# Performance work log

Measured on AMD Instinct MI355X. Metric: run time of the kernel, lower is better.

Reference implementation:

```python
import jax, jax.numpy as jnp
import numpy as np

COMMITMENT_COST = 0.25


def setup_inputs() -> dict:
    key = jax.random.key(0)
    k1, k2 = jax.random.split(key)
    z_e = jax.random.normal(k1, (32, 64, 64, 64), dtype=jnp.float32)  # [B, C, H, W]
    emb = jax.random.normal(k2, (1024, 64), dtype=jnp.float32)        # [K, D] codebook
    return {"z_e": z_e, "emb": emb}


def reference(z_e, emb):
    B, C, H, W = z_e.shape
    K, D = emb.shape
    # [B, C, H, W] -> [B, H, W, C] -> [N, D]
    z = jnp.transpose(z_e, (0, 2, 3, 1))
    z_flat = z.reshape(-1, D)
    # squared L2 distances: ||z||^2 + ||e||^2 - 2 z e^T  -> [N, K]
    distances = (jnp.sum(z_flat * z_flat, axis=1, keepdims=True)
                 + jnp.sum(emb * emb, axis=1)
                 - 2.0 * (z_flat @ emb.T))
    indices = jnp.argmin(distances, axis=1)               # [N]
    encodings = jax.nn.one_hot(indices, K, dtype=z_flat.dtype)  # [N, K]
    quantized = emb[indices].reshape(z.shape)             # [B, H, W, D]
    # commitment loss (codebook is frozen / EMA-updated, so quantized is detached)
    loss = COMMITMENT_COST * jnp.mean((jax.lax.stop_gradient(quantized) - z) ** 2)
    # straight-through estimator
    quantized_st = z + jax.lax.stop_gradient(quantized - z)
    avg_probs = jnp.mean(encodings, axis=0)               # [K]
    perplexity = jnp.exp(-jnp.sum(avg_probs * jnp.log(avg_probs + 1e-10)))
    out = jnp.transpose(quantized_st, (0, 3, 1, 2))       # back to [B, C, H, W]
    return out, loss, perplexity, encodings
```

## Files before the change

kernel.cpp:

```cpp
#include <hip/hip_runtime.h>

typedef __attribute__((ext_vector_type(8)))  __bf16 bf16x8;
typedef __attribute__((ext_vector_type(16))) float  f32x16;

#define NPTS   131072
#define KCODES 1024
#define DDIM   64
#define HWSZ   4096

#define LOSS_OFF    8388608
#define PERP_OFF    8388609
#define ENC_OFF     8388610

#define IMG_BYTES   25600
#define HIST_OFF    409600
#define BLOSS_OFF   413696
#define WS_NEED     415744

#define GLOBAL_AS __attribute__((address_space(1)))
#define LDS_AS    __attribute__((address_space(3)))

__device__ __forceinline__ unsigned rnhi(float x) {
    unsigned u = __float_as_uint(x);
    return (u + 0x7fffu + ((u >> 16) & 1u)) & 0xffff0000u;
}

__device__ __forceinline__ void split3(float x, unsigned short& h1, unsigned short& h2, unsigned short& h3) {
    unsigned a = rnhi(x); float r1 = x - __uint_as_float(a);
    unsigned b = rnhi(r1); float r2 = r1 - __uint_as_float(b);
    unsigned c = rnhi(r2);
    h1 = (unsigned short)(a >> 16);
    h2 = (unsigned short)(b >> 16);
    h3 = (unsigned short)(c >> 16);
}

__global__ __launch_bounds__(256) void prep_kernel(const float* __restrict__ emb,
                                                   uint4* __restrict__ planes,
                                                   int* __restrict__ hist) {
    const int k = blockIdx.x * 256 + threadIdx.x;
    hist[k] = 0;
    float row[DDIM];
    const float4* r = (const float4*)(emb + (size_t)k * DDIM);
    float s0 = 0.f, s1 = 0.f, s2 = 0.f, s3 = 0.f;
#pragma unroll
    for (int i = 0; i < 16; ++i) {
        float4 v = r[i];
        row[4 * i + 0] = v.x; row[4 * i + 1] = v.y;
        row[4 * i + 2] = v.z; row[4 * i + 3] = v.w;
        s0 = fmaf(v.x, v.x, s0);
        s1 = fmaf(v.y, v.y, s1);
        s2 = fmaf(v.z, v.z, s2);
        s3 = fmaf(v.w, v.w, s3);
    }
    const float e2v = (s0 + s1) + (s2 + s3);

    const int c  = k >> 6, lc = k & 63;
    uint4* img = planes + (size_t)c * (IMG_BYTES / 16);
#pragma unroll
    for (int sl = 0; sl < 8; ++sl) {
        unsigned w1[4], w2[4], w3[4];
#pragma unroll
        for (int m = 0; m < 4; ++m) {
            unsigned short a0, b0, c0, a1, b1, c1;
            split3(-2.f * row[sl * 8 + 2 * m    ], a0, b0, c0);
            split3(-2.f * row[sl * 8 + 2 * m + 1], a1, b1, c1);
            w1[m] = (unsigned)a0 | ((unsigned)a1 << 16);
            w2[m] = (unsigned)b0 | ((unsigned)b1 << 16);
            w3[m] = (unsigned)c0 | ((unsigned)c1 << 16);
        }
        img[0 * 512 + sl * 64 + lc] = make_uint4(w1[0], w1[1], w1[2], w1[3]);
        img[1 * 512 + sl * 64 + lc] = make_uint4(w2[0], w2[1], w2[2], w2[3]);
        img[2 * 512 + sl * 64 + lc] = make_uint4(w3[0], w3[1], w3[2], w3[3]);
    }
    {
        unsigned short s1e, s2e, s3e;
        split3(e2v, s1e, s2e, s3e);
        img[1536 + lc] = make_uint4((unsigned)s1e | ((unsigned)s2e << 16), (unsigned)s3e, 0u, 0u);
    }
}

__global__ __launch_bounds__(512, 4) void vq_fused(
    const float* __restrict__ z_e, const char* __restrict__ planesg,
    const float* __restrict__ emb, float* __restrict__ out,
    float* __restrict__ enc, int* __restrict__ hist,
    float* __restrict__ blockLoss)
{
    __shared__ __align__(16) char sbuf[2][IMG_BYTES];
    __shared__ int   sidx[256];
    __shared__ float swsum[8];

    const int tid  = threadIdx.x, bid = blockIdx.x;
    const int lane = tid & 63,    wid = tid >> 6;
    const int hi   = lane >> 5,   col = lane & 31;

    {
#pragma unroll
        for (int i = 0; i < 4; ++i) {
            const int seg = wid + 8 * i;
            if (seg < 25) {
                const char* g = planesg + seg * 1024 + lane * 16;
                __builtin_amdgcn_global_load_lds((const GLOBAL_AS void*)g,
                                                 (LDS_AS void*)(&sbuf[0][0] + seg * 1024), 16, 0, 0);
            }
        }
    }

    float* encSlice = enc + (size_t)bid * 256 * KCODES;
    float4* encF4   = (float4*)(encSlice + 2);

    const int n  = bid * 256 + wid * 32 + col;
    const int b  = n >> 12, hw = n & (HWSZ - 1);
    const float* zp = z_e + (size_t)b * (DDIM * HWSZ) + hw;

    bf16x8 Bv0[4], Bv1[4], Bv2[4];
    float zzp = 0.f;
#pragma unroll
    for (int kk = 0; kk < 4; ++kk) {
        union { unsigned u[4]; bf16x8 v; } p1, p2, p3;
#pragma unroll
        for (int m = 0; m < 4; ++m) {
            float x0 = zp[(size_t)(16 * kk + 8 * hi + 2 * m    ) * HWSZ];
            float x1 = zp[(size_t)(16 * kk + 8 * hi + 2 * m + 1) * HWSZ];
            zzp = fmaf(x0, x0, zzp);
            zzp = fmaf(x1, x1, zzp);
            unsigned short a0, b0, c0, a1, b1, c1;
            split3(x0, a0, b0, c0);
            split3(x1, a1, b1, c1);
            p1.u[m] = (unsigned)a0 | ((unsigned)a1 << 16);
            p2.u[m] = (unsigned)b0 | ((unsigned)b1 << 16);
            p3.u[m] = (unsigned)c0 | ((unsigned)c1 << 16);
        }
        Bv0[kk] = p1.v; Bv1[kk] = p2.v; Bv2[kk] = p3.v;
    }

    bf16x8 Bone;
    {
        union { unsigned u[4]; bf16x8 v; } o;
        o.u[0] = hi ? 0u : 0x3F803F80u;
        o.u[1] = hi ? 0u : 0x00003F80u;
        o.u[2] = 0u; o.u[3] = 0u;
        Bone = o.v;
    }

    __syncthreads();

    float best = 3.4e38f;
    int   bestk = 0;
    const float4 z4 = make_float4(0.f, 0.f, 0.f, 0.f);

    for (int c = 0; c < 16; ++c) {
        const int cur = c & 1;
        if (c + 1 < 16) {
            const char* gimg = planesg + (size_t)(c + 1) * IMG_BYTES;
#pragma unroll
            for (int i = 0; i < 4; ++i) {
                const int seg = wid + 8 * i;
                if (seg < 25) {
                    __builtin_amdgcn_global_load_lds((const GLOBAL_AS void*)(gimg + seg * 1024 + lane * 16),
                                                     (LDS_AS void*)(&sbuf[1 - cur][0] + seg * 1024), 16, 0, 0);
                }
            }
        }
        {
            const int base = c * 4096 + tid;
#pragma unroll
            for (int j = 0; j < 8; ++j) {
                const int idx = base + j * 512;
                if (idx < 65535) encF4[idx] = z4;
            }
            if (c == 0) {
                if (tid == 0) *(float2*)encSlice = make_float2(0.f, 0.f);
                if (tid == 1) *(float2*)(encSlice + 262142) = make_float2(0.f, 0.f);
            }
        }

        const char* img = &sbuf[cur][0];
#pragma unroll
        for (int t = 0; t < 2; ++t) {
            const int rowoff = (32 * t + col) * 16;
            f32x16 acc = {0.f,0.f,0.f,0.f,0.f,0.f,0.f,0.f,0.f,0.f,0.f,0.f,0.f,0.f,0.f,0.f};
            bf16x8 eA = *(const bf16x8*)(img + 24576 + rowoff);
            acc = __builtin_amdgcn_mfma_f32_32x32x16_bf16(eA, Bone, acc, 0, 0, 0);
#pragma unroll
            for (int kk = 0; kk < 4; ++kk) {
                const char* bse = img + (2 * kk + hi) * 1024 + rowoff;
                bf16x8 a1 = *(const bf16x8*)(bse);
                bf16x8 a2 = *(const bf16x8*)(bse + 8192);
                acc = __builtin_amdgcn_mfma_f32_32x32x16_bf16(a1, Bv0[kk], acc, 0, 0, 0);
                acc = __builtin_amdgcn_mfma_f32_32x32x16_bf16(a2, Bv0[kk], acc, 0, 0, 0);
                acc = __builtin_amdgcn_mfma_f32_32x32x16_bf16(a1, Bv1[kk], acc, 0, 0, 0);
                acc = __builtin_amdgcn_mfma_f32_32x32x16_bf16(a2, Bv1[kk], acc, 0, 0, 0);
                bf16x8 a3 = *(const bf16x8*)(bse + 16384);
                acc = __builtin_amdgcn_mfma_f32_32x32x16_bf16(a3, Bv0[kk], acc, 0, 0, 0);
                acc = __builtin_amdgcn_mfma_f32_32x32x16_bf16(a1, Bv2[kk], acc, 0, 0, 0);
            }
            const int cbase = c * 64 + 32 * t + 4 * hi;
#pragma unroll
            for (int r = 0; r < 16; ++r) {
                const int code = cbase + (r & 3) + 8 * (r >> 2);
                const float sc = acc[r];
                if (sc < best) { best = sc; bestk = code; }
            }
        }
        __syncthreads();
    }

    float obest = __shfl_down(best, 32);
    int   oidx  = __shfl_down(bestk, 32);
    float ozz   = __shfl_down(zzp, 32);
    if (obest < best || (obest == best && oidx < bestk)) { best = obest; bestk = oidx; }
    const float zz = zzp + ozz;
    float contrib = (lane < 32) ? (best + zz) : 0.f;
    if (lane < 32) {
        sidx[wid * 32 + col] = bestk;
        atomicAdd(&hist[bestk], 1);
    }
#pragma unroll
    for (int off = 32; off > 0; off >>= 1) contrib += __shfl_down(contrib, off);
    if (lane == 0) swsum[wid] = contrib;
    __syncthreads();
    if (tid == 0) {
        float s = 0.f;
        for (int i = 0; i < 8; ++i) s += swsum[i];
        blockLoss[bid] = s;
    }

    if (lane < 32) {
        const int nn = bid * 256 + wid * 32 + col;
        enc[(size_t)nn * KCODES + bestk] = 1.0f;
    }

    {
        const int i  = tid & 255, c0 = (tid >> 8) * 32;
        const int k  = sidx[i];
        const int nn = bid * 256 + i, bb = nn >> 12, hh = nn & (HWSZ - 1);
        const float4* er = (const float4*)(emb + (size_t)k * DDIM + c0);
        float* ob = out + (size_t)bb * (DDIM * HWSZ) + hh;
#pragma unroll
        for (int m = 0; m < 8; ++m) {
            float4 q = er[m];
            ob[(size_t)(c0 + 4 * m    ) * HWSZ] = q.x;
            ob[(size_t)(c0 + 4 * m + 1) * HWSZ] = q.y;
            ob[(size_t)(c0 + 4 * m + 2) * HWSZ] = q.z;
            ob[(size_t)(c0 + 4 * m + 3) * HWSZ] = q.w;
        }
    }
}

__global__ __launch_bounds__(256) void e2_kernel(const float* __restrict__ emb,
                                                 float* __restrict__ e2,
                                                 int* __restrict__ hist) {
    int k = blockIdx.x * 256 + threadIdx.x;
    hist[k] = 0;
    const float4* r = (const float4*)(emb + (size_t)k * DDIM);
    float s0 = 0.f, s1 = 0.f, s2 = 0.f, s3 = 0.f;
#pragma unroll
    for (int i = 0; i < 16; ++i) {
        float4 v = r[i];
        s0 = fmaf(v.x, v.x, s0);
        s1 = fmaf(v.y, v.y, s1);
        s2 = fmaf(v.z, v.z, s2);
        s3 = fmaf(v.w, v.w, s3);
    }
    e2[k] = (s0 + s1) + (s2 + s3);
}

__global__ __launch_bounds__(512, 4) void vq_mfma(
    const float* __restrict__ z_e, const float* __restrict__ emb,
    const float* __restrict__ e2g, float* __restrict__ out,
    float* __restrict__ enc, int* __restrict__ hist,
    float* __restrict__ blockLoss)
{
    __shared__ unsigned short planeA[3 * 8 * 1024];
    __shared__ float se2[KCODES];
    __shared__ int   sidx[256];
    __shared__ float swsum[8];

    const int tid  = threadIdx.x, bid = blockIdx.x;
    const int lane = tid & 63,    wid = tid >> 6;
    const int hi   = lane >> 5,   col = lane & 31;

    for (int i = tid; i < KCODES; i += 512) se2[i] = e2g[i];

    float* encSlice = enc + (size_t)bid * 256 * KCODES;
    float4* encF4   = (float4*)(encSlice + 2);

    const int n  = bid * 256 + wid * 32 + col;
    const int b  = n >> 12, hw = n & (HWSZ - 1);
    const float* zp = z_e + (size_t)b * (DDIM * HWSZ) + hw;

    bf16x8 Bv[3][4];
    float zzp = 0.f;
#pragma unroll
    for (int kk = 0; kk < 4; ++kk) {
        union { unsigned u[4]; bf16x8 v; } p1, p2, p3;
#pragma unroll
        for (int m = 0; m < 4; ++m) {
            float x0 = zp[(size_t)(16 * kk + 8 * hi + 2 * m    ) * HWSZ];
            float x1 = zp[(size_t)(16 * kk + 8 * hi + 2 * m + 1) * HWSZ];
            zzp = fmaf(x0, x0, zzp);
            zzp = fmaf(x1, x1, zzp);
            unsigned short a0, b0, c0, a1, b1, c1;
            split3(x0, a0, b0, c0);
            split3(x1, a1, b1, c1);
            p1.u[m] = (unsigned)a0 | ((unsigned)a1 << 16);
            p2.u[m] = (unsigned)b0 | ((unsigned)b1 << 16);
            p3.u[m] = (unsigned)c0 | ((unsigned)c1 << 16);
        }
        Bv[0][kk] = p1.v; Bv[1][kk] = p2.v; Bv[2][kk] = p3.v;
    }

    float best = 3.4e38f;
    int   bestk = 0;

    for (int chunk = 0; chunk < 8; ++chunk) {
        __syncthreads();
#pragma unroll
        for (int it = 0; it < 2; ++it) {
            const int code = tid & 127;
            const int sl   = (tid >> 7) + 4 * it;
            const float4* ep = (const float4*)(emb + (size_t)(chunk * 128 + code) * DDIM + sl * 8);
            float4 va = ep[0], vb = ep[1];
            float xs[8] = {va.x, va.y, va.z, va.w, vb.x, vb.y, vb.z, vb.w};
            unsigned w1[4], w2[4], w3[4];
#pragma unroll
            for (int m = 0; m < 4; ++m) {
                unsigned short a0, b0, c0, a1, b1, c1;
                split3(-2.f * xs[2 * m    ], a0, b0, c0);
                split3(-2.f * xs[2 * m + 1], a1, b1, c1);
                w1[m] = (unsigned)a0 | ((unsigned)a1 << 16);
                w2[m] = (unsigned)b0 | ((unsigned)b1 << 16);
                w3[m] = (unsigned)c0 | ((unsigned)c1 << 16);
            }
            const int off = sl * 1024 + code * 8;
            *(uint4*)&planeA[0 * 8192 + off] = make_uint4(w1[0], w1[1], w1[2], w1[3]);
            *(uint4*)&planeA[1 * 8192 + off] = make_uint4(w2[0], w2[1], w2[2], w2[3]);
            *(uint4*)&planeA[2 * 8192 + off] = make_uint4(w3[0], w3[1], w3[2], w3[3]);
        }
        __syncthreads();

        {
            const float4 z4 = make_float4(0.f, 0.f, 0.f, 0.f);
            const int base = chunk * 8192 + tid;
#pragma unroll
            for (int it = 0; it < 16; ++it) {
                const int idx = base + it * 512;
                if (idx < 65535) encF4[idx] = z4;
            }
            if (chunk == 0) {
                if (tid == 0) *(float2*)encSlice = make_float2(0.f, 0.f);
                if (tid == 1) *(float2*)(encSlice + 262142) = make_float2(0.f, 0.f);
            }
        }

        for (int t = 0; t < 4; ++t) {
            f32x16 acc0 = {0.f,0.f,0.f,0.f,0.f,0.f,0.f,0.f,0.f,0.f,0.f,0.f,0.f,0.f,0.f,0.f};
            f32x16 acc1 = {0.f,0.f,0.f,0.f,0.f,0.f,0.f,0.f,0.f,0.f,0.f,0.f,0.f,0.f,0.f,0.f};
            const int arow = (32 * t + col) * 8;
#pragma unroll
            for (int kk = 0; kk < 4; ++kk) {
                const int sb = (2 * kk + hi) * 1024 + arow;
                bf16x8 a1 = *(const bf16x8*)&planeA[0 * 8192 + sb];
                bf16x8 a2 = *(const bf16x8*)&planeA[1 * 8192 + sb];
                bf16x8 a3 = *(const bf16x8*)&planeA[2 * 8192 + sb];
                acc0 = __builtin_amdgcn_mfma_f32_32x32x16_bf16(a1, Bv[0][kk], acc0, 0, 0, 0);
                acc1 = __builtin_amdgcn_mfma_f32_32x32x16_bf16(a1, Bv[1][kk], acc1, 0, 0, 0);
                acc0 = __builtin_amdgcn_mfma_f32_32x32x16_bf16(a2, Bv[0][kk], acc0, 0, 0, 0);
                acc1 = __builtin_amdgcn_mfma_f32_32x32x16_bf16(a2, Bv[1][kk], acc1, 0, 0, 0);
                acc0 = __builtin_amdgcn_mfma_f32_32x32x16_bf16(a1, Bv[2][kk], acc0, 0, 0, 0);
                acc1 = __builtin_amdgcn_mfma_f32_32x32x16_bf16(a3, Bv[0][kk], acc1, 0, 0, 0);
                acc0 = __builtin_amdgcn_mfma_f32_32x32x16_bf16(a2, Bv[2][kk], acc0, 0, 0, 0);
                acc1 = __builtin_amdgcn_mfma_f32_32x32x16_bf16(a3, Bv[1][kk], acc1, 0, 0, 0);
            }
            const int cbase = chunk * 128 + 32 * t + 4 * hi;
#pragma unroll
            for (int r = 0; r < 16; ++r) {
                const int row  = (r & 3) + 8 * (r >> 2);
                const int code = cbase + row;
                const float sc = (acc0[r] + acc1[r]) + se2[code];
                if (sc < best) { best = sc; bestk = code; }
            }
        }
    }

    float obest = __shfl_down(best, 32);
    int   oidx  = __shfl_down(bestk, 32);
    float ozz   = __shfl_down(zzp, 32);
    if (obest < best || (obest == best && oidx < bestk)) { best = obest; bestk = oidx; }
    const float zz = zzp + ozz;
    float contrib = (lane < 32) ? (best + zz) : 0.f;
    if (lane < 32) {
        sidx[wid * 32 + col] = bestk;
        atomicAdd(&hist[bestk], 1);
    }
#pragma unroll
    for (int off = 32; off > 0; off >>= 1) contrib += __shfl_down(contrib, off);
    if (lane == 0) swsum[wid] = contrib;
    __syncthreads();
    if (tid == 0) {
        float s = 0.f;
        for (int i = 0; i < 8; ++i) s += swsum[i];
        blockLoss[bid] = s;
    }

    if (lane < 32) {
        const int nn = bid * 256 + wid * 32 + col;
        enc[(size_t)nn * KCODES + bestk] = 1.0f;
    }

    {
        const int i  = tid & 255, c0 = (tid >> 8) * 32;
        const int k  = sidx[i];
        const int nn = bid * 256 + i, bb = nn >> 12, hh = nn & (HWSZ - 1);
        const float4* er = (const float4*)(emb + (size_t)k * DDIM + c0);
        float* ob = out + (size_t)bb * (DDIM * HWSZ) + hh;
#pragma unroll
        for (int m = 0; m < 8; ++m) {
            float4 q = er[m];
            ob[(size_t)(c0 + 4 * m    ) * HWSZ] = q.x;
            ob[(size_t)(c0 + 4 * m + 1) * HWSZ] = q.y;
            ob[(size_t)(c0 + 4 * m + 2) * HWSZ] = q.z;
            ob[(size_t)(c0 + 4 * m + 3) * HWSZ] = q.w;
        }
    }
}

__global__ __launch_bounds__(1024) void fin_kernel(const int* __restrict__ hist,
                                                   const float* __restrict__ blockLoss,
                                                   float* __restrict__ dout)
{
    __shared__ float redE[16];
    __shared__ float redL[16];
    const int t = threadIdx.x;

    float p = (float)hist[t] * (1.f / 131072.f);
    float term = p * logf(p + 1e-10f);
    float lv = (t < 512) ? blockLoss[t] : 0.f;
#pragma unroll
    for (int off = 32; off > 0; off >>= 1) {
        term += __shfl_down(term, off);
        lv   += __shfl_down(lv, off);
    }
    const int lane = t & 63, wid = t >> 6;
    if (lane == 0) { redE[wid] = term; redL[wid] = lv; }
    __syncthreads();
    if (t == 0) {
        float te = 0.f, tl = 0.f;
        for (int i = 0; i < 16; ++i) { te += redE[i]; tl += redL[i]; }
        dout[LOSS_OFF] = 0.25f * tl * (1.f / (131072.f * 64.f));
        dout[PERP_OFF] = expf(-te);
    }
}

extern "C" void kernel_launch(void* const* d_in, const int* in_sizes, int n_in,
                              void* d_out, int out_size, void* d_ws, size_t ws_size,
                              hipStream_t stream) {
    const float* z_e = (const float*)d_in[0];
    const float* emb = (const float*)d_in[1];
    float* out = (float*)d_out;
    float* enc = out + ENC_OFF;

    if (ws_size >= (size_t)WS_NEED) {
        uint4* planes    = (uint4*)d_ws;
        int*   hist      = (int*)((char*)d_ws + HIST_OFF);
        float* blockLoss = (float*)((char*)d_ws + BLOSS_OFF);
        prep_kernel<<<4, 256, 0, stream>>>(emb, planes, hist);
        vq_fused<<<NPTS / 256, 512, 0, stream>>>(z_e, (const char*)d_ws, emb,
                                                 out, enc, hist, blockLoss);
        fin_kernel<<<1, 1024, 0, stream>>>(hist, blockLoss, out);
    } else {
        float* e2        = (float*)d_ws;
        int*   hist      = (int*)((char*)d_ws + 4096);
        float* blockLoss = (float*)((char*)d_ws + 8192);
        e2_kernel<<<4, 256, 0, stream>>>(emb, e2, hist);
        vq_mfma<<<NPTS / 256, 512, 0, stream>>>(z_e, emb, e2, out, enc, hist, blockLoss);
        fin_kernel<<<1, 1024, 0, stream>>>(hist, blockLoss, out);
    }
}
```

Baseline: 163.3 us.

## Move one-hot zero-fill into dedicated blocks and add a scatter pass

The grid grows to 768 blocks, and every third block only zero-fills a strided group of encoding rows, skipping the first two floats of each row. Compute blocks no longer interleave zero stores with the MFMA distance loop. Instead they write their argmin index as an int into the first slot of the row. A new small kernel then reads that index, writes the first two floats and sets the one-hot 1.0. The goal is to separate the large write of the encodings matrix from the compute so the two run concurrently on different blocks, at the cost of an extra kernel launch and a dependent read/write of each row.

```diff
diff --git a/kernel.cpp b/kernel.cpp
--- a/kernel.cpp
+++ b/kernel.cpp
@@ -89,9 +89,31 @@
     __shared__ int   sidx[256];
     __shared__ float swsum[8];
 
-    const int tid  = threadIdx.x, bid = blockIdx.x;
+    const int tid  = threadIdx.x;
+    const int rbid = blockIdx.x;
     const int lane = tid & 63,    wid = tid >> 6;
-    const int hi   = lane >> 5,   col = lane & 31;
+
+    if ((rbid % 3) == 2) {
+        const int zid = rbid / 3;
+        const float4 z4 = make_float4(0.f, 0.f, 0.f, 0.f);
+        for (int g = 0; g < 8; ++g) {
+            float* reg = enc + (size_t)(zid + 256 * g) * 65536;
+            for (int rr = wid; rr < 64; rr += 8) {
+                float* rowp = reg + rr * 1024;
+                float4* rp4 = (float4*)(rowp + 2);
+#pragma unroll
+                for (int p = 0; p < 4; ++p) {
+                    const int idx = p * 64 + lane;
+                    if (idx < 255) rp4[idx] = z4;
+                }
+                if (lane == 63) *(float2*)(rowp + 1022) = make_float2(0.f, 0.f);
+            }
+        }
+        return;
+    }
+
+    const int bid = (rbid / 3) * 2 + (rbid % 3);
+    const int hi  = lane >> 5, col = lane & 31;
 
     {
 #pragma unroll
@@ -104,9 +126,6 @@
             }
         }
     }
-
-    float* encSlice = enc + (size_t)bid * 256 * KCODES;
-    float4* encF4   = (float4*)(encSlice + 2);
 
     const int n  = bid * 256 + wid * 32 + col;
     const int b  = n >> 12, hw = n & (HWSZ - 1);
@@ -146,7 +165,6 @@
 
     float best = 3.4e38f;
     int   bestk = 0;
-    const float4 z4 = make_float4(0.f, 0.f, 0.f, 0.f);
 
     for (int c = 0; c < 16; ++c) {
         const int cur = c & 1;
@@ -159,18 +177,6 @@
                     __builtin_amdgcn_global_load_lds((const GLOBAL_AS void*)(gimg + seg * 1024 + lane * 16),
                                                      (LDS_AS void*)(&sbuf[1 - cur][0] + seg * 1024), 16, 0, 0);
                 }
-            }
-        }
-        {
-            const int base = c * 4096 + tid;
-#pragma unroll
-            for (int j = 0; j < 8; ++j) {
-                const int idx = base + j * 512;
-                if (idx < 65535) encF4[idx] = z4;
-            }
-            if (c == 0) {
-                if (tid == 0) *(float2*)encSlice = make_float2(0.f, 0.f);
-                if (tid == 1) *(float2*)(encSlice + 262142) = make_float2(0.f, 0.f);
             }
         }
 
@@ -214,6 +220,7 @@
     if (lane < 32) {
         sidx[wid * 32 + col] = bestk;
         atomicAdd(&hist[bestk], 1);
+        ((int*)enc)[(size_t)n * KCODES] = bestk;
     }
 #pragma unroll
     for (int off = 32; off > 0; off >>= 1) contrib += __shfl_down(contrib, off);
@@ -225,11 +232,6 @@
         blockLoss[bid] = s;
     }
 
-    if (lane < 32) {
-        const int nn = bid * 256 + wid * 32 + col;
-        enc[(size_t)nn * KCODES + bestk] = 1.0f;
-    }
-
     {
         const int i  = tid & 255, c0 = (tid >> 8) * 32;
         const int k  = sidx[i];
@@ -245,6 +247,14 @@
             ob[(size_t)(c0 + 4 * m + 3) * HWSZ] = q.w;
         }
     }
+}
+
+__global__ __launch_bounds__(256) void scatter_kernel(float* __restrict__ enc) {
+    const int n = blockIdx.x * 256 + threadIdx.x;
+    float* rowp = enc + (size_t)n * KCODES;
+    const int k = *(const int*)rowp;
+    *(float2*)rowp = make_float2(k == 0 ? 1.f : 0.f, k == 1 ? 1.f : 0.f);
+    if (k >= 2) rowp[k] = 1.0f;
 }
 
 __global__ __launch_bounds__(256) void e2_kernel(const float* __restrict__ emb,
@@ -465,8 +475,9 @@
         int*   hist      = (int*)((char*)d_ws + HIST_OFF);
         float* blockLoss = (float*)((char*)d_ws + BLOSS_OFF);
         prep_kernel<<<4, 256, 0, stream>>>(emb, planes, hist);
-        vq_fused<<<NPTS / 256, 512, 0, stream>>>(z_e, (const char*)d_ws, emb,
-                                                 out, enc, hist, blockLoss);
+        vq_fused<<<768, 512, 0, stream>>>(z_e, (const char*)d_ws, emb,
+                                          out, enc, hist, blockLoss);
+        scatter_kernel<<<NPTS / 256, 256, 0, stream>>>(enc);
         fin_kernel<<<1, 1024, 0, stream>>>(hist, blockLoss, out);
     } else {
         float* e2        = (float*)d_ws;
```

Result: slower. 206.0 us (+26.2%).
